# Performance work log

Measured on AMD Instinct MI355X. Metric: run time of the kernel, lower is better.

Reference implementation:

```python
import jax, jax.numpy as jnp
import numpy as np

# Module constants (match init_kwargs)
G = 8        # number of channel groups (len(list_input_dim))
D = 16       # per-group input dim
L = 1024     # sequence length
B = 16       # batch
E = 8        # num_experts
OUT = 64     # out_channels
KS = 3       # emb_kernel_size
K = 4        # hardcoded self.k in Channel_Embedding
LOSS_COEF = 0.01


def setup_inputs() -> dict:
    key = jax.random.key(0)
    k0, k1, k2, k3 = jax.random.split(key, 4)
    x = jax.random.normal(k0, (B, G * D, L), jnp.float32)
    # torch inits w_gate to zeros (degenerate); use small random weights for meaningful routing
    w_gate = jax.random.normal(k1, (G, D * 5, E), jnp.float32) * 0.1
    conv1_w = jax.random.normal(k2, (G, OUT, D, KS), jnp.float32) * (1.0 / np.sqrt(D * KS))
    conv1_b = jnp.zeros((G, OUT), jnp.float32)
    conv2_w = jax.random.normal(k3, (G, OUT * E, OUT, 1), jnp.float32) * (1.0 / np.sqrt(OUT))
    conv2_b = jnp.zeros((G, OUT * E), jnp.float32)
    return dict(x=x, w_gate=w_gate, conv1_w=conv1_w, conv1_b=conv1_b,
                conv2_w=conv2_w, conv2_b=conv2_b)


def _cv_squared(v):
    # torch: x.float().var() (unbiased) / (mean^2 + eps)
    v = v.astype(jnp.float32)
    return jnp.var(v, ddof=1) / (jnp.mean(v) ** 2 + 1e-10)


def _conv1d(x, w, b):
    # x [B,C,L], w [O,I,K] -> [B,O,L'] (VALID, stride 1)
    y = jax.lax.conv_general_dilated(x, w, (1,), 'VALID',
                                     dimension_numbers=('NCH', 'OIH', 'NCH'))
    return y + b[None, :, None]


def _group_forward(xg, wg, c1w, c1b, c2w, c2b):
    # xg: [B, D, L] single channel group
    Bb = xg.shape[0]
    # gating input: last timesteps [-6:-1] -> [B, D*5]
    gate_in = xg[:, :, -6:-1].reshape(Bb, -1)
    logits = jax.nn.softmax(gate_in @ wg, axis=1)           # [B, E]
    top_v, top_i = jax.lax.top_k(logits, min(K + 1, E))     # [B, K+1]
    tkv, tki = top_v[:, :K], top_i[:, :K]
    gk = tkv / (tkv.sum(1, keepdims=True) + 1e-6)
    gates = jnp.zeros_like(logits).at[jnp.arange(Bb)[:, None], tki].set(gk)  # [B, E]
    load = (gates > 0).sum(0)                               # eval path: _gates_to_load
    loss = _cv_squared(gates.sum(0)) + _cv_squared(load)
    # experts: conv(D->OUT, k=KS) -> tanh -> conv(OUT -> OUT*E, k=1)
    h = jnp.tanh(_conv1d(xg, c1w, c1b))
    raw = _conv1d(h, c2w, c2b)                              # [B, OUT*E, L']
    Lp = raw.shape[-1]
    # channel index = d*E + e (matches torch permute+reshape(B,-1,OUT,E))
    moe = jnp.einsum('bdel,be->bdl', raw.reshape(Bb, OUT, E, Lp), gates)  # [B, OUT, L']
    return moe, loss, gates


def reference(x, w_gate, conv1_w, conv1_b, conv2_w, conv2_b):
    # split channels into G groups of D: [G, B, D, L]
    xg = x.reshape(x.shape[0], G, D, x.shape[-1]).transpose(1, 0, 2, 3)
    moe, loss, gates = jax.vmap(_group_forward)(xg, w_gate, conv1_w, conv1_b, conv2_w, conv2_b)
    combine_features = moe.transpose(1, 0, 2, 3)   # [B, G, OUT, L']
    out_loss = LOSS_COEF * loss.sum()
    gates_out = gates.transpose(1, 2, 0)           # [B, E, G]
    return combine_features, out_loss, gates_out
```

## Files before the change

kernel.cpp:

```cpp
#include <hip/hip_runtime.h>
#include <hip/hip_bf16.h>

#define NG   8
#define ND   16
#define NL   1024
#define NB   16
#define NE   8
#define NOUT 64
#define NKS  3
#define NK   4
#define NLP  1022

#define OUT_LOSS  (NB*NG*NOUT*NLP)
#define OUT_GATES (OUT_LOSS + 1)

typedef short bf16x8 __attribute__((ext_vector_type(8)));
typedef float f32x4  __attribute__((ext_vector_type(4)));

#define MFMA16(A, B, C) __builtin_amdgcn_mfma_f32_16x16x32_bf16((A), (B), (C), 0, 0, 0)

__device__ __forceinline__ float tanh_fast(float x) {
    float e = exp2f(x * 2.885390081777927f);
    return 1.0f - 2.0f / (e + 1.0f);
}

__device__ __forceinline__ unsigned fbits(float a) { return __builtin_bit_cast(unsigned, a); }
__device__ __forceinline__ float resid(float a) {
    return a - __builtin_bit_cast(float, fbits(a) & 0xFFFF0000u);
}
__device__ __forceinline__ int pack2(float a, float b) {
    return (int)((fbits(a) >> 16) | (fbits(b) & 0xFFFF0000u));
}

__device__ __forceinline__ void compute_gates_f(
    const float* __restrict__ x, const float* __restrict__ wg,
    int g, int b, float gates[8])
{
    float gi[80];
    const float* xrow = x + (size_t)(b * 128 + g * 16) * 1024 + (1024 - 6);
    #pragma unroll
    for (int d = 0; d < 16; ++d) {
        #pragma unroll
        for (int tt = 0; tt < 5; ++tt) gi[d * 5 + tt] = xrow[d * 1024 + tt];
    }
    float lg[8];
    #pragma unroll
    for (int e = 0; e < 8; ++e) lg[e] = 0.f;
    const float* wgg = wg + g * 640;
    #pragma unroll
    for (int j = 0; j < 80; ++j) {
        const float v = gi[j];
        #pragma unroll
        for (int e = 0; e < 8; ++e) lg[e] = fmaf(v, wgg[j * 8 + e], lg[e]);
    }
    float mx = lg[0];
    #pragma unroll
    for (int e = 1; e < 8; ++e) mx = fmaxf(mx, lg[e]);
    float s = 0.f;
    #pragma unroll
    for (int e = 0; e < 8; ++e) { lg[e] = expf(lg[e] - mx); s += lg[e]; }
    const float invsm = 1.f / s;
    #pragma unroll
    for (int e = 0; e < 8; ++e) lg[e] *= invsm;

    int used = 0;
    float tv[4]; int ti[4];
    #pragma unroll
    for (int k = 0; k < 4; ++k) {
        float bv = -1.f; int be = 0;
        #pragma unroll
        for (int e = 0; e < 8; ++e) {
            if (!((used >> e) & 1) && lg[e] > bv) { bv = lg[e]; be = e; }
        }
        tv[k] = bv; ti[k] = be; used |= (1 << be);
    }
    const float s4 = tv[0] + tv[1] + tv[2] + tv[3];
    const float invs = 1.f / (s4 + 1e-6f);
    #pragma unroll
    for (int e = 0; e < 8; ++e) {
        float v = 0.f;
        #pragma unroll
        for (int k = 0; k < 4; ++k) if (ti[k] == e) v = tv[k] * invs;
        gates[e] = v;
    }
}

__global__ __launch_bounds__(256) void prep_kernel(
    const float* __restrict__ x,   const float* __restrict__ wg,
    const float* __restrict__ c1w, const float* __restrict__ c2w,
    const float* __restrict__ c2b,
    float* __restrict__ out, int4* __restrict__ weffA,
    float* __restrict__ beff, int4* __restrict__ w1fA)
{
    const int bid = blockIdx.x;
    const int t   = threadIdx.x;

    __shared__ float glds[128][8];
    __shared__ float impa[64], loda[64];
    __shared__ float lossg[8];

    if (bid < 128) {
        const int gb = bid, g = gb >> 4, b = gb & 15;
        float gt[8];
        compute_gates_f(x, wg, g, b, gt);

        const int o  = t >> 2;
        const int iq = (t & 3) * 16;
        const float* w2g = c2w + (size_t)g * 512 * 64 + (size_t)o * 8 * 64 + iq;
        float acc[16];
        #pragma unroll
        for (int q = 0; q < 16; ++q) acc[q] = 0.f;
        #pragma unroll
        for (int e = 0; e < 8; ++e) {
            const float4* src = (const float4*)(w2g + e * 64);
            #pragma unroll
            for (int q = 0; q < 4; ++q) {
                float4 v = src[q];
                acc[q*4+0] = fmaf(gt[e], v.x, acc[q*4+0]);
                acc[q*4+1] = fmaf(gt[e], v.y, acc[q*4+1]);
                acc[q*4+2] = fmaf(gt[e], v.z, acc[q*4+2]);
                acc[q*4+3] = fmaf(gt[e], v.w, acc[q*4+3]);
            }
        }
        const int mt  = o >> 4;
        const int ks  = iq >> 5;
        const int lgA = (iq & 31) >> 3;
        int4* wdst = weffA + gb * 1024 + mt * 128 + ks * 64;
        #pragma unroll
        for (int R = 0; R < 2; ++R) {
            int4 whi, wlo;
            whi.x = pack2(acc[R*8+0], acc[R*8+1]);
            whi.y = pack2(acc[R*8+2], acc[R*8+3]);
            whi.z = pack2(acc[R*8+4], acc[R*8+5]);
            whi.w = pack2(acc[R*8+6], acc[R*8+7]);
            wlo.x = pack2(resid(acc[R*8+0]), resid(acc[R*8+1]));
            wlo.y = pack2(resid(acc[R*8+2]), resid(acc[R*8+3]));
            wlo.z = pack2(resid(acc[R*8+4]), resid(acc[R*8+5]));
            wlo.w = pack2(resid(acc[R*8+6]), resid(acc[R*8+7]));
            const int slot = (lgA + R) * 16 + (o & 15);
            wdst[slot]       = whi;
            wdst[512 + slot] = wlo;
        }
        if (t < 64) {
            const float* b2g = c2b + g * 512;
            float a = 0.f;
            #pragma unroll
            for (int e = 0; e < 8; ++e) a = fmaf(gt[e], b2g[t * 8 + e], a);
            beff[gb * 64 + t] = a;
        }
    } else if (bid < 136) {
        const int g = bid - 128;
        for (int u = t; u < 1024; u += 256) {
            const int s    = u >> 9;
            const int mt   = (u >> 7) & 3;
            const int ks   = (u >> 6) & 1;
            const int lgrp = (u >> 4) & 3;
            const int m    = u & 15;
            const int o    = mt * 16 + m;
            float v[8];
            #pragma unroll
            for (int e = 0; e < 8; ++e) {
                const int k = ks * 32 + lgrp * 8 + e;
                if (k < 48) {
                    const int tap = (k < 32) ? (k >> 4) : 2;
                    const int i   = k & 15;
                    const float w = c1w[((size_t)(g * 64 + o) * 16 + i) * 3 + tap];
                    v[e] = (s == 0) ? w : resid(w);
                } else v[e] = 0.f;
            }
            int4 pk;
            pk.x = pack2(v[0], v[1]); pk.y = pack2(v[2], v[3]);
            pk.z = pack2(v[4], v[5]); pk.w = pack2(v[6], v[7]);
            w1fA[(size_t)g * 1024 + u] = pk;
        }
    } else {
        float gates[8];
        const int g = t >> 4, b = t & 15;
        if (t < 128) {
            compute_gates_f(x, wg, g, b, gates);
            #pragma unroll
            for (int e = 0; e < 8; ++e) {
                glds[t][e] = gates[e];
                out[OUT_GATES + (b * 8 + e) * 8 + g] = gates[e];
            }
        }
        __syncthreads();
        if (t < 64) {
            const int gg = t >> 3, e = t & 7;
            float si = 0.f, sl = 0.f;
            for (int bb = 0; bb < 16; ++bb) {
                const float v = glds[gg * 16 + bb][e];
                si += v;
                sl += (v > 0.f) ? 1.f : 0.f;
            }
            impa[t] = si; loda[t] = sl;
        }
        __syncthreads();
        if (t < 8) {
            float m1 = 0.f, m2 = 0.f;
            #pragma unroll
            for (int e = 0; e < 8; ++e) { m1 += impa[t * 8 + e]; m2 += loda[t * 8 + e]; }
            m1 *= 0.125f; m2 *= 0.125f;
            float v1 = 0.f, v2 = 0.f;
            #pragma unroll
            for (int e = 0; e < 8; ++e) {
                const float d1 = impa[t * 8 + e] - m1, d2 = loda[t * 8 + e] - m2;
                v1 += d1 * d1; v2 += d2 * d2;
            }
            v1 *= (1.f / 7.f); v2 *= (1.f / 7.f);
            lossg[t] = v1 / (m1 * m1 + 1e-10f) + v2 / (m2 * m2 + 1e-10f);
        }
        __syncthreads();
        if (t == 0) {
            float tot = 0.f;
            #pragma unroll
            for (int gg = 0; gg < 8; ++gg) tot += lossg[gg];
            out[OUT_LOSS] = 0.01f * tot;
        }
    }
}

__global__ __launch_bounds__(256, 4) void main_kernel(
    const float* __restrict__ x,    const int4* __restrict__ w1fA,
    const float* __restrict__ b1,   const int4* __restrict__ weffA,
    const float* __restrict__ beff, float* __restrict__ out)
{
    __shared__ int4 hfrag[2048];
    float* xtileT = (float*)hfrag;

    const int bid  = blockIdx.x;
    const int xcd  = bid & 7;
    const int jj   = bid >> 3;
    const int gb   = ((jj & 15) << 3) | xcd;
    const int tile = jj >> 4;
    const int g    = gb >> 4, b = gb & 15;
    const int t    = threadIdx.x;
    const int lane = t & 63;
    const int wv   = t >> 6;
    const int col  = lane & 15;
    const int j4   = lane >> 4;
    const int l0   = tile * 128;

    {
        const int si  = t >> 4;
        const int sc0 = t & 15;
        const float* xr = x + (size_t)(b * 128 + g * 16 + si) * 1024;
        #pragma unroll
        for (int kk = 0; kk < 9; ++kk) {
            const int c = sc0 + kk * 16;
            if (c < 130) {
                int gc = l0 + c; if (gc > 1023) gc = 1023;
                xtileT[c * 20 + si] = xr[gc];
            }
        }
    }
    __syncthreads();

    bf16x8 B1h[2][2], B1l[2][2];
    #pragma unroll
    for (int tl = 0; tl < 2; ++tl) {
        #pragma unroll
        for (int ks = 0; ks < 2; ++ks) {
            const int tap = (ks == 0) ? (j4 >> 1) : 2;
            const int i0  = (j4 & 1) * 8;
            const bool valid = (ks == 0) || (j4 < 2);
            const int c = (wv * 2 + tl) * 16 + col;
            const float* p = &xtileT[(c + tap) * 20 + i0];
            float v[8];
            *(float4*)&v[0] = *(const float4*)p;
            *(float4*)&v[4] = *(const float4*)(p + 4);
            #pragma unroll
            for (int e = 0; e < 8; ++e) if (!valid) v[e] = 0.f;
            int4 bh, bl;
            bh.x = pack2(v[0], v[1]); bh.y = pack2(v[2], v[3]);
            bh.z = pack2(v[4], v[5]); bh.w = pack2(v[6], v[7]);
            bl.x = pack2(resid(v[0]), resid(v[1])); bl.y = pack2(resid(v[2]), resid(v[3]));
            bl.z = pack2(resid(v[4]), resid(v[5])); bl.w = pack2(resid(v[6]), resid(v[7]));
            B1h[tl][ks] = __builtin_bit_cast(bf16x8, bh);
            B1l[tl][ks] = __builtin_bit_cast(bf16x8, bl);
        }
    }
    __syncthreads();

    const int rbase = j4 << 2;
    f32x4 acc1[2][4];
    #pragma unroll
    for (int mt = 0; mt < 4; ++mt) {
        f32x4 bv = *(const f32x4*)(b1 + g * 64 + mt * 16 + rbase);
        acc1[0][mt] = bv; acc1[1][mt] = bv;
    }
    const int4* w1base = w1fA + g * 1024 + lane;
    #pragma unroll
    for (int mt = 0; mt < 4; ++mt) {
        bf16x8 Ah0 = *(const bf16x8*)(w1base + mt * 128);
        bf16x8 Ah1 = *(const bf16x8*)(w1base + mt * 128 + 64);
        bf16x8 Al0 = *(const bf16x8*)(w1base + 512 + mt * 128);
        bf16x8 Al1 = *(const bf16x8*)(w1base + 512 + mt * 128 + 64);
        #pragma unroll
        for (int tl = 0; tl < 2; ++tl) {
            f32x4 a = acc1[tl][mt];
            a = MFMA16(Ah0, B1h[tl][0], a);
            a = MFMA16(Ah0, B1l[tl][0], a);
            a = MFMA16(Al0, B1h[tl][0], a);
            a = MFMA16(Ah1, B1h[tl][1], a);
            a = MFMA16(Ah1, B1l[tl][1], a);
            a = MFMA16(Al1, B1h[tl][1], a);
            acc1[tl][mt] = a;
        }
    }

    {
        char* base = (char*)hfrag;
        const int wb  = wv * 512;
        const int lgt0 = j4 >> 1;
        const int woff = (j4 & 1) * 8;
        #pragma unroll
        for (int tl = 0; tl < 2; ++tl) {
            #pragma unroll
            for (int mt = 0; mt < 4; ++mt) {
                const float t0 = tanh_fast(acc1[tl][mt][0]);
                const float t1 = tanh_fast(acc1[tl][mt][1]);
                const float t2 = tanh_fast(acc1[tl][mt][2]);
                const float t3 = tanh_fast(acc1[tl][mt][3]);
                const int kst = mt >> 1;
                const int lgt = ((mt & 1) << 1) + lgt0;
                const int uhi = wb + kst * 128 + tl * 64 + lgt * 16 + col;
                uint2 whi, wlo;
                whi.x = (unsigned)pack2(t0, t1);
                whi.y = (unsigned)pack2(t2, t3);
                wlo.x = (unsigned)pack2(resid(t0), resid(t1));
                wlo.y = (unsigned)pack2(resid(t2), resid(t3));
                *(uint2*)(base + uhi * 16 + woff)         = whi;
                *(uint2*)(base + (uhi + 256) * 16 + woff) = wlo;
            }
        }
    }

    f32x4 acc2[4][2];
    const float* befp = beff + gb * 64 + rbase;
    #pragma unroll
    for (int mt = 0; mt < 4; ++mt) {
        f32x4 bv = *(const f32x4*)(befp + mt * 16);
        acc2[mt][0] = bv; acc2[mt][1] = bv;
    }
    const int4* wAbase = weffA + gb * 1024 + lane;
    #pragma unroll
    for (int ks = 0; ks < 2; ++ks) {
        const int wb = wv * 512;
        bf16x8 Bh0 = *(const bf16x8*)&hfrag[wb + ks * 128 + lane];
        bf16x8 Bh1 = *(const bf16x8*)&hfrag[wb + ks * 128 + 64 + lane];
        bf16x8 Bl0 = *(const bf16x8*)&hfrag[wb + (2 + ks) * 128 + lane];
        bf16x8 Bl1 = *(const bf16x8*)&hfrag[wb + (2 + ks) * 128 + 64 + lane];
        #pragma unroll
        for (int mt = 0; mt < 4; ++mt) {
            bf16x8 Ah = *(const bf16x8*)(wAbase + mt * 128 + ks * 64);
            bf16x8 Al = *(const bf16x8*)(wAbase + 512 + mt * 128 + ks * 64);
            acc2[mt][0] = MFMA16(Ah, Bh0, acc2[mt][0]);
            acc2[mt][1] = MFMA16(Ah, Bh1, acc2[mt][1]);
            acc2[mt][0] = MFMA16(Ah, Bl0, acc2[mt][0]);
            acc2[mt][1] = MFMA16(Ah, Bl1, acc2[mt][1]);
            acc2[mt][0] = MFMA16(Al, Bh0, acc2[mt][0]);
            acc2[mt][1] = MFMA16(Al, Bh1, acc2[mt][1]);
        }
    }

    const int colg = l0 + wv * 32 + col;
    float* outg = out + (size_t)((b * 8 + g) * 64) * NLP;
    #pragma unroll
    for (int mt = 0; mt < 4; ++mt) {
        #pragma unroll
        for (int tl = 0; tl < 2; ++tl) {
            const int cg = colg + tl * 16;
            if (cg < NLP) {
                float* orow = outg + (size_t)(mt * 16 + rbase) * NLP + cg;
                orow[0]             = acc2[mt][tl][0];
                orow[(size_t)NLP]   = acc2[mt][tl][1];
                orow[(size_t)NLP*2] = acc2[mt][tl][2];
                orow[(size_t)NLP*3] = acc2[mt][tl][3];
            }
        }
    }
}

extern "C" void kernel_launch(void* const* d_in, const int* in_sizes, int n_in,
                              void* d_out, int out_size, void* d_ws, size_t ws_size,
                              hipStream_t stream) {
    const float* x   = (const float*)d_in[0];
    const float* wg  = (const float*)d_in[1];
    const float* c1w = (const float*)d_in[2];
    const float* c1b = (const float*)d_in[3];
    const float* c2w = (const float*)d_in[4];
    const float* c2b = (const float*)d_in[5];
    float* out = (float*)d_out;

    char* ws    = (char*)d_ws;
    int4* weffA = (int4*)ws;
    int4* w1fA  = weffA + 131072;
    float* beff = (float*)(w1fA + 8192);

    prep_kernel<<<137, 256, 0, stream>>>(x, wg, c1w, c2w, c2b, out, weffA, beff, w1fA);
    main_kernel<<<1024, 256, 0, stream>>>(x, w1fA, c1b, weffA, beff, out);
}
```

Before: 110.6 us.

## Pre-split x tile into bf16 hi/lo in LDS and process column tiles sequentially

The x tile is now converted to bf16 hi/lo pairs once, during the global-to-LDS staging, and laid out so MFMA B fragments load directly as int4. The two 16-column subtiles per wave are processed one at a time through conv1, tanh, conv2 and store, rather than both at once. This halves the accumulator and fragment registers and the h-fragment LDS buffer, aiming at lower register pressure and fewer conversion instructions. In exchange the weight fragments are reloaded for each subtile, and the split now uses round-to-nearest bf16 conversion instead of truncation.

```diff
diff --git a/kernel.cpp b/kernel.cpp
--- a/kernel.cpp
+++ b/kernel.cpp
@@ -30,6 +30,13 @@
 }
 __device__ __forceinline__ int pack2(float a, float b) {
     return (int)((fbits(a) >> 16) | (fbits(b) & 0xFFFF0000u));
+}
+__device__ __forceinline__ unsigned short bfb(float v) {
+    __hip_bfloat16 h = __float2bfloat16(v);
+    return __builtin_bit_cast(unsigned short, h);
+}
+__device__ __forceinline__ float bff(unsigned short s) {
+    return __builtin_bit_cast(float, ((unsigned)s) << 16);
 }
 
 __device__ __forceinline__ void compute_gates_f(
@@ -225,8 +232,8 @@
     const float* __restrict__ b1,   const int4* __restrict__ weffA,
     const float* __restrict__ beff, float* __restrict__ out)
 {
-    __shared__ int4 hfrag[2048];
-    float* xtileT = (float*)hfrag;
+    __shared__ int4 hfrag[1024];
+    __shared__ char xs[130 * 80 + 16];
 
     const int bid  = blockIdx.x;
     const int xcd  = bid & 7;
@@ -240,143 +247,128 @@
     const int col  = lane & 15;
     const int j4   = lane >> 4;
     const int l0   = tile * 128;
+    const int wb   = wv * 256;
 
     {
         const int si  = t >> 4;
         const int sc0 = t & 15;
         const float* xr = x + (size_t)(b * 128 + g * 16 + si) * 1024;
+        const int boff = (si >> 3) * 32 + (si & 7) * 2;
         #pragma unroll
         for (int kk = 0; kk < 9; ++kk) {
             const int c = sc0 + kk * 16;
             if (c < 130) {
                 int gc = l0 + c; if (gc > 1023) gc = 1023;
-                xtileT[c * 20 + si] = xr[gc];
+                const float v = xr[gc];
+                const unsigned short hs = bfb(v);
+                const unsigned short ls = bfb(v - bff(hs));
+                *(unsigned short*)(xs + c * 80 + boff)      = hs;
+                *(unsigned short*)(xs + c * 80 + boff + 16) = ls;
             }
         }
     }
     __syncthreads();
 
-    bf16x8 B1h[2][2], B1l[2][2];
+    const int4*  w1base = w1fA + g * 1024 + lane;
+    const int4*  wAbase = weffA + gb * 1024 + lane;
+    const int    rbase  = j4 << 2;
+    float* outg = out + (size_t)((b * 8 + g) * 64) * NLP;
+
     #pragma unroll
     for (int tl = 0; tl < 2; ++tl) {
-        #pragma unroll
-        for (int ks = 0; ks < 2; ++ks) {
-            const int tap = (ks == 0) ? (j4 >> 1) : 2;
-            const int i0  = (j4 & 1) * 8;
-            const bool valid = (ks == 0) || (j4 < 2);
-            const int c = (wv * 2 + tl) * 16 + col;
-            const float* p = &xtileT[(c + tap) * 20 + i0];
-            float v[8];
-            *(float4*)&v[0] = *(const float4*)p;
-            *(float4*)&v[4] = *(const float4*)(p + 4);
-            #pragma unroll
-            for (int e = 0; e < 8; ++e) if (!valid) v[e] = 0.f;
-            int4 bh, bl;
-            bh.x = pack2(v[0], v[1]); bh.y = pack2(v[2], v[3]);
-            bh.z = pack2(v[4], v[5]); bh.w = pack2(v[6], v[7]);
-            bl.x = pack2(resid(v[0]), resid(v[1])); bl.y = pack2(resid(v[2]), resid(v[3]));
-            bl.z = pack2(resid(v[4]), resid(v[5])); bl.w = pack2(resid(v[6]), resid(v[7]));
-            B1h[tl][ks] = __builtin_bit_cast(bf16x8, bh);
-            B1l[tl][ks] = __builtin_bit_cast(bf16x8, bl);
-        }
-    }
-    __syncthreads();
-
-    const int rbase = j4 << 2;
-    f32x4 acc1[2][4];
-    #pragma unroll
-    for (int mt = 0; mt < 4; ++mt) {
-        f32x4 bv = *(const f32x4*)(b1 + g * 64 + mt * 16 + rbase);
-        acc1[0][mt] = bv; acc1[1][mt] = bv;
-    }
-    const int4* w1base = w1fA + g * 1024 + lane;
-    #pragma unroll
-    for (int mt = 0; mt < 4; ++mt) {
-        bf16x8 Ah0 = *(const bf16x8*)(w1base + mt * 128);
-        bf16x8 Ah1 = *(const bf16x8*)(w1base + mt * 128 + 64);
-        bf16x8 Al0 = *(const bf16x8*)(w1base + 512 + mt * 128);
-        bf16x8 Al1 = *(const bf16x8*)(w1base + 512 + mt * 128 + 64);
-        #pragma unroll
-        for (int tl = 0; tl < 2; ++tl) {
-            f32x4 a = acc1[tl][mt];
-            a = MFMA16(Ah0, B1h[tl][0], a);
-            a = MFMA16(Ah0, B1l[tl][0], a);
-            a = MFMA16(Al0, B1h[tl][0], a);
-            a = MFMA16(Ah1, B1h[tl][1], a);
-            a = MFMA16(Ah1, B1l[tl][1], a);
-            a = MFMA16(Al1, B1h[tl][1], a);
-            acc1[tl][mt] = a;
-        }
-    }
-
-    {
-        char* base = (char*)hfrag;
-        const int wb  = wv * 512;
-        const int lgt0 = j4 >> 1;
-        const int woff = (j4 & 1) * 8;
-        #pragma unroll
-        for (int tl = 0; tl < 2; ++tl) {
+        const int nloc = (wv * 2 + tl) * 16 + col;
+        bf16x8 xBh0, xBl0, xBh1, xBl1;
+        {
+            const char* p0 = xs + (nloc + (j4 >> 1)) * 80 + (j4 & 1) * 32;
+            int4 bh = *(const int4*)p0;
+            int4 bl = *(const int4*)(p0 + 16);
+            xBh0 = __builtin_bit_cast(bf16x8, bh);
+            xBl0 = __builtin_bit_cast(bf16x8, bl);
+            const char* p1 = xs + (nloc + 2) * 80 + (j4 & 1) * 32;
+            int4 ch_ = *(const int4*)p1;
+            int4 cl_ = *(const int4*)(p1 + 16);
+            if (j4 >= 2) {
+                ch_.x = ch_.y = ch_.z = ch_.w = 0;
+                cl_.x = cl_.y = cl_.z = cl_.w = 0;
+            }
+            xBh1 = __builtin_bit_cast(bf16x8, ch_);
+            xBl1 = __builtin_bit_cast(bf16x8, cl_);
+        }
+
+        f32x4 acc1[4];
+        #pragma unroll
+        for (int mt = 0; mt < 4; ++mt)
+            acc1[mt] = *(const f32x4*)(b1 + g * 64 + mt * 16 + rbase);
+        #pragma unroll
+        for (int mt = 0; mt < 4; ++mt) {
+            bf16x8 Ah0 = *(const bf16x8*)(w1base + mt * 128);
+            bf16x8 Ah1 = *(const bf16x8*)(w1base + mt * 128 + 64);
+            bf16x8 Al0 = *(const bf16x8*)(w1base + 512 + mt * 128);
+            bf16x8 Al1 = *(const bf16x8*)(w1base + 512 + mt * 128 + 64);
+            f32x4 a = acc1[mt];
+            a = MFMA16(Ah0, xBh0, a);
+            a = MFMA16(Ah0, xBl0, a);
+            a = MFMA16(Al0, xBh0, a);
+            a = MFMA16(Ah1, xBh1, a);
+            a = MFMA16(Ah1, xBl1, a);
+            a = MFMA16(Al1, xBh1, a);
+            acc1[mt] = a;
+        }
+
+        {
+            char* base = (char*)hfrag;
+            const int woff = (j4 & 1) * 8;
+            const int lgt0 = j4 >> 1;
             #pragma unroll
             for (int mt = 0; mt < 4; ++mt) {
-                const float t0 = tanh_fast(acc1[tl][mt][0]);
-                const float t1 = tanh_fast(acc1[tl][mt][1]);
-                const float t2 = tanh_fast(acc1[tl][mt][2]);
-                const float t3 = tanh_fast(acc1[tl][mt][3]);
+                const float t0 = tanh_fast(acc1[mt][0]);
+                const float t1 = tanh_fast(acc1[mt][1]);
+                const float t2 = tanh_fast(acc1[mt][2]);
+                const float t3 = tanh_fast(acc1[mt][3]);
+                const unsigned short h0 = bfb(t0), h1 = bfb(t1);
+                const unsigned short h2 = bfb(t2), h3 = bfb(t3);
+                uint2 whi, wlo;
+                whi.x = (unsigned)h0 | ((unsigned)h1 << 16);
+                whi.y = (unsigned)h2 | ((unsigned)h3 << 16);
+                wlo.x = (unsigned)bfb(t0 - bff(h0)) | ((unsigned)bfb(t1 - bff(h1)) << 16);
+                wlo.y = (unsigned)bfb(t2 - bff(h2)) | ((unsigned)bfb(t3 - bff(h3)) << 16);
                 const int kst = mt >> 1;
                 const int lgt = ((mt & 1) << 1) + lgt0;
-                const int uhi = wb + kst * 128 + tl * 64 + lgt * 16 + col;
-                uint2 whi, wlo;
-                whi.x = (unsigned)pack2(t0, t1);
-                whi.y = (unsigned)pack2(t2, t3);
-                wlo.x = (unsigned)pack2(resid(t0), resid(t1));
-                wlo.y = (unsigned)pack2(resid(t2), resid(t3));
-                *(uint2*)(base + uhi * 16 + woff)         = whi;
-                *(uint2*)(base + (uhi + 256) * 16 + woff) = wlo;
-            }
-        }
-    }
-
-    f32x4 acc2[4][2];
-    const float* befp = beff + gb * 64 + rbase;
-    #pragma unroll
-    for (int mt = 0; mt < 4; ++mt) {
-        f32x4 bv = *(const f32x4*)(befp + mt * 16);
-        acc2[mt][0] = bv; acc2[mt][1] = bv;
-    }
-    const int4* wAbase = weffA + gb * 1024 + lane;
-    #pragma unroll
-    for (int ks = 0; ks < 2; ++ks) {
-        const int wb = wv * 512;
-        bf16x8 Bh0 = *(const bf16x8*)&hfrag[wb + ks * 128 + lane];
-        bf16x8 Bh1 = *(const bf16x8*)&hfrag[wb + ks * 128 + 64 + lane];
-        bf16x8 Bl0 = *(const bf16x8*)&hfrag[wb + (2 + ks) * 128 + lane];
-        bf16x8 Bl1 = *(const bf16x8*)&hfrag[wb + (2 + ks) * 128 + 64 + lane];
-        #pragma unroll
-        for (int mt = 0; mt < 4; ++mt) {
-            bf16x8 Ah = *(const bf16x8*)(wAbase + mt * 128 + ks * 64);
-            bf16x8 Al = *(const bf16x8*)(wAbase + 512 + mt * 128 + ks * 64);
-            acc2[mt][0] = MFMA16(Ah, Bh0, acc2[mt][0]);
-            acc2[mt][1] = MFMA16(Ah, Bh1, acc2[mt][1]);
-            acc2[mt][0] = MFMA16(Ah, Bl0, acc2[mt][0]);
-            acc2[mt][1] = MFMA16(Ah, Bl1, acc2[mt][1]);
-            acc2[mt][0] = MFMA16(Al, Bh0, acc2[mt][0]);
-            acc2[mt][1] = MFMA16(Al, Bh1, acc2[mt][1]);
-        }
-    }
-
-    const int colg = l0 + wv * 32 + col;
-    float* outg = out + (size_t)((b * 8 + g) * 64) * NLP;
-    #pragma unroll
-    for (int mt = 0; mt < 4; ++mt) {
-        #pragma unroll
-        for (int tl = 0; tl < 2; ++tl) {
-            const int cg = colg + tl * 16;
-            if (cg < NLP) {
+                const int u   = wb + kst * 64 + lgt * 16 + col;
+                *(uint2*)(base + u * 16 + woff)           = whi;
+                *(uint2*)(base + (u + 128) * 16 + woff)   = wlo;
+            }
+        }
+
+        f32x4 acc2[4];
+        #pragma unroll
+        for (int mt = 0; mt < 4; ++mt)
+            acc2[mt] = *(const f32x4*)(beff + gb * 64 + mt * 16 + rbase);
+        #pragma unroll
+        for (int ks = 0; ks < 2; ++ks) {
+            bf16x8 Bh = *(const bf16x8*)&hfrag[wb + ks * 64 + lane];
+            bf16x8 Bl = *(const bf16x8*)&hfrag[wb + 128 + ks * 64 + lane];
+            #pragma unroll
+            for (int mt = 0; mt < 4; ++mt) {
+                bf16x8 Ah = *(const bf16x8*)(wAbase + mt * 128 + ks * 64);
+                bf16x8 Al = *(const bf16x8*)(wAbase + 512 + mt * 128 + ks * 64);
+                f32x4 a = acc2[mt];
+                a = MFMA16(Ah, Bh, a);
+                a = MFMA16(Ah, Bl, a);
+                a = MFMA16(Al, Bh, a);
+                acc2[mt] = a;
+            }
+        }
+
+        const int cg = l0 + nloc;
+        if (cg < NLP) {
+            #pragma unroll
+            for (int mt = 0; mt < 4; ++mt) {
                 float* orow = outg + (size_t)(mt * 16 + rbase) * NLP + cg;
-                orow[0]             = acc2[mt][tl][0];
-                orow[(size_t)NLP]   = acc2[mt][tl][1];
-                orow[(size_t)NLP*2] = acc2[mt][tl][2];
-                orow[(size_t)NLP*3] = acc2[mt][tl][3];
+                orow[0]             = acc2[mt][0];
+                orow[(size_t)NLP]   = acc2[mt][1];
+                orow[(size_t)NLP*2] = acc2[mt][2];
+                orow[(size_t)NLP*3] = acc2[mt][3];
             }
         }
     }
```

Result: slower. 113.2 us (+2.3%).
